# Kernel tuning notes

Hardware: AMD Instinct MI355X
Metric: run time of the kernel (lower is better)

## Reference

```python
import jax, jax.numpy as jnp
import numpy as np

KERNEL = (3, 3, 3)
STRIDE = (1, 1, 1)
PAD = (1, 1, 1)
DIL = (1, 1, 1)


def setup_inputs() -> dict:
    key = jax.random.key(0)
    k1, k2 = jax.random.split(key)
    # input: [B, C, D, H, W]
    x = jax.random.normal(k1, (2, 64, 16, 64, 64), dtype=jnp.float32)
    # per-pixel weights: [B, heads, weight_channels, kernel_volume, D_out, H_out, W_out]
    weight = jax.random.normal(k2, (2, 1, 16, 27, 16, 64, 64), dtype=jnp.float32)
    return {"x": x, "weight": weight}


def _aggregate(x, weight):
    # involution-style 3D local aggregation with zero padding.
    B, C, D, H, W = x.shape
    _, heads, wc, kvol, Do, Ho, Wo = weight.shape
    kd, kh, kw = KERNEL
    assert kvol == kd * kh * kw and C % wc == 0
    Q = C // wc  # channel-sharing groups: channel c uses weight channel c % wc
    xp = jnp.pad(x, ((0, 0), (0, 0), (PAD[0], PAD[0]), (PAD[1], PAD[1]), (PAD[2], PAD[2])))
    # channels laid out so that c = q*wc + r -> weight channel r == c % wc
    out = jnp.zeros((B, heads, Q, wc, Do, Ho, Wo), dtype=x.dtype)
    for ikd in range(kd):
        for ikh in range(kh):
            for ikw in range(kw):  # fixed small structural loop (27 taps)
                k = (ikd * kh + ikh) * kw + ikw
                d0 = ikd * DIL[0]
                h0 = ikh * DIL[1]
                w0 = ikw * DIL[2]
                x_k = xp[:, :,
                         d0:d0 + (Do - 1) * STRIDE[0] + 1:STRIDE[0],
                         h0:h0 + (Ho - 1) * STRIDE[1] + 1:STRIDE[1],
                         w0:w0 + (Wo - 1) * STRIDE[2] + 1:STRIDE[2]]
                x_k = x_k.reshape(B, Q, wc, Do, Ho, Wo)
                # [B,1,Q,wc,Do,Ho,Wo] * [B,heads,1,wc,Do,Ho,Wo]
                out = out + x_k[:, None] * weight[:, :, None, :, k]
    return out.reshape(B, heads * C, Do, Ho, Wo)


def reference(x, weight):
    return _aggregate(x, weight)
```

## Files before the change

kernel.cpp:

```cpp
#include <hip/hip_runtime.h>


#define D_DIM 16
#define NQ 4
#define RS 68

typedef float f4_t __attribute__((ext_vector_type(4)));

__global__ __launch_bounds__(256) void lconv_kernel(
    const float* __restrict__ x, const float* __restrict__ wt, float* __restrict__ out)
{
    __shared__ __align__(16) float lds[2][NQ][18][RS];

    const int tid = threadIdx.x;
    const int tw  = tid & 15;
    const int th  = tid >> 4;

    int bid = blockIdx.x;
    const int ho_tile = bid & 3;  bid >>= 2;
    const int dout    = bid & 15; bid >>= 4;
    const int c       = bid & 15; bid >>= 4;
    const int b       = bid;

    const int ho_base = ho_tile * 16;
    const int ho  = ho_base + th;
    const int wo0 = tw * 4;
    const int lw  = (tw == 0) ? 65 : (wo0 - 1);

    {
        float* l0 = &lds[0][0][0][0];
        for (int i = tid; i < 2 * NQ * 18 * 4; i += 256) {
            const int word = 64 + (i & 3);
            const int idx  = i >> 2;
            l0[(size_t)idx * RS + word] = 0.f;
        }
        const int oob_h = (ho_tile == 0) ? 0 : (ho_tile == 3) ? 17 : -1;
        if (oob_h >= 0) {
            for (int i = tid; i < 2 * NQ * RS; i += 256) {
                const int bq = i / RS, w = i - bq * RS;
                l0[((size_t)bq * 18 + oob_h) * RS + w] = 0.f;
            }
        }
    }

    const float* xbase = x + ((size_t)(b * 64 + c) * 16) * 4096;

    auto stage = [&](int buf, int d) {
        const float* src = xbase + (size_t)d * 4096;
        for (int i = tid; i < 72 * 16; i += 256) {
            const int row = i >> 4;
            const int seg = i & 15;
            const int q   = row / 18;
            const int hl  = row - q * 18;
            const int gh  = ho_base - 1 + hl;
            if ((unsigned)gh < 64u) {
                const f4_t v = *reinterpret_cast<const f4_t*>(
                    src + (size_t)q * 1048576 + (size_t)gh * 64 + seg * 4);
                *reinterpret_cast<f4_t*>(&lds[buf][q][hl][seg * 4]) = v;
            }
        }
    };

    float acc[NQ][4];
    #pragma unroll
    for (int q = 0; q < NQ; ++q)
        #pragma unroll
        for (int j = 0; j < 4; ++j) acc[q][j] = 0.f;

    const float* wbase = wt + (((size_t)(b * 16 + c) * 27) * 16 + dout) * 4096
                            + (size_t)ho * 64 + wo0;

    if (dout - 1 >= 0) stage(0, dout - 1);
    __syncthreads();

    #pragma unroll
    for (int dd = 0; dd < 3; ++dd) {
        const int cur = dd & 1, nxt = cur ^ 1;
        const int dn = dout + dd;
        if (dd < 2 && dn < D_DIM) stage(nxt, dn);

        const int d = dout + dd - 1;
        if ((unsigned)d < (unsigned)D_DIM) {
            #pragma unroll
            for (int dh = 0; dh < 3; ++dh) {
                float xv[NQ][6];
                #pragma unroll
                for (int q = 0; q < NQ; ++q) {
                    const float* r = &lds[cur][q][th + dh][0];
                    const f4_t m = *reinterpret_cast<const f4_t*>(r + wo0);
                    xv[q][0] = r[lw];
                    xv[q][1] = m.x; xv[q][2] = m.y; xv[q][3] = m.z; xv[q][4] = m.w;
                    xv[q][5] = r[wo0 + 4];
                }
                #pragma unroll
                for (int dw = 0; dw < 3; ++dw) {
                    const int k = (dd * 3 + dh) * 3 + dw;
                    const f4_t w4 = __builtin_nontemporal_load(
                        reinterpret_cast<const f4_t*>(wbase + (size_t)k * 65536));
                    #pragma unroll
                    for (int q = 0; q < NQ; ++q) {
                        acc[q][0] = fmaf(xv[q][0 + dw], w4.x, acc[q][0]);
                        acc[q][1] = fmaf(xv[q][1 + dw], w4.y, acc[q][1]);
                        acc[q][2] = fmaf(xv[q][2 + dw], w4.z, acc[q][2]);
                        acc[q][3] = fmaf(xv[q][3 + dw], w4.w, acc[q][3]);
                    }
                }
            }
        }
        __syncthreads();
    }

    #pragma unroll
    for (int q = 0; q < NQ; ++q) {
        float* orow = out + ((size_t)(b * 64 + q * 16 + c) * 16 + dout) * 4096
                          + (size_t)ho * 64 + wo0;
        f4_t r; r.x = acc[q][0]; r.y = acc[q][1]; r.z = acc[q][2]; r.w = acc[q][3];
        __builtin_nontemporal_store(r, reinterpret_cast<f4_t*>(orow));
    }
}

extern "C" void kernel_launch(void* const* d_in, const int* in_sizes, int n_in,
                              void* d_out, int out_size, void* d_ws, size_t ws_size,
                              hipStream_t stream) {
    const float* x  = (const float*)d_in[0];
    const float* wt = (const float*)d_in[1];
    float* out      = (float*)d_out;

    dim3 grid(2048), block(256);
    hipLaunchKernelGGL(lconv_kernel, grid, block, 0, stream, x, wt, out);
}
```

Measured before the change: 59.49 us.

## Process four output depths per block with ring-buffered async LDS staging

Each block now computes four consecutive output depth slices, staging input depth planes into a four-slot LDS ring so each plane is loaded once and reused across three output depths. Staging uses global_load_lds async copies, and out-of-range rows and depths read from a zeroed workspace page set by a memset before launch. This cuts the grid from 2048 to 512 blocks and roughly halves redundant input loads, but it lowers the number of resident waves available to hide the dominant per-pixel weight streaming, and it adds a memset to each launch.

```diff
diff --git a/kernel.cpp b/kernel.cpp
--- a/kernel.cpp
+++ b/kernel.cpp
@@ -1,16 +1,24 @@
 #include <hip/hip_runtime.h>
+#include <stdint.h>
 
 
-#define D_DIM 16
 #define NQ 4
-#define RS 68
-
 typedef float f4_t __attribute__((ext_vector_type(4)));
 
+#define BUF_FLOATS (4 * 18 * 64)
+#define LDS_FLOATS (64 + 4 * BUF_FLOATS + 64)
+
+__device__ __forceinline__ void async_copy16(const float* gsrc, float* ldst) {
+    __builtin_amdgcn_global_load_lds(
+        (const __attribute__((address_space(1))) uint32_t*)gsrc,
+        (__attribute__((address_space(3))) uint32_t*)ldst, 16, 0, 0);
+}
+
 __global__ __launch_bounds__(256) void lconv_kernel(
-    const float* __restrict__ x, const float* __restrict__ wt, float* __restrict__ out)
+    const float* __restrict__ x, const float* __restrict__ wt, float* __restrict__ out,
+    const float* __restrict__ zp)
 {
-    __shared__ __align__(16) float lds[2][NQ][18][RS];
+    __shared__ float lds_raw[LDS_FLOATS];
 
     const int tid = threadIdx.x;
     const int tw  = tid & 15;
@@ -18,79 +26,71 @@
 
     int bid = blockIdx.x;
     const int ho_tile = bid & 3;  bid >>= 2;
-    const int dout    = bid & 15; bid >>= 4;
+    const int a       = bid & 3;  bid >>= 2;
     const int c       = bid & 15; bid >>= 4;
     const int b       = bid;
 
     const int ho_base = ho_tile * 16;
     const int ho  = ho_base + th;
     const int wo0 = tw * 4;
-    const int lw  = (tw == 0) ? 65 : (wo0 - 1);
-
-    {
-        float* l0 = &lds[0][0][0][0];
-        for (int i = tid; i < 2 * NQ * 18 * 4; i += 256) {
-            const int word = 64 + (i & 3);
-            const int idx  = i >> 2;
-            l0[(size_t)idx * RS + word] = 0.f;
-        }
-        const int oob_h = (ho_tile == 0) ? 0 : (ho_tile == 3) ? 17 : -1;
-        if (oob_h >= 0) {
-            for (int i = tid; i < 2 * NQ * RS; i += 256) {
-                const int bq = i / RS, w = i - bq * RS;
-                l0[((size_t)bq * 18 + oob_h) * RS + w] = 0.f;
-            }
-        }
-    }
+    const int d0  = a * 4;
 
     const float* xbase = x + ((size_t)(b * 64 + c) * 16) * 4096;
 
-    auto stage = [&](int buf, int d) {
-        const float* src = xbase + (size_t)d * 4096;
-        for (int i = tid; i < 72 * 16; i += 256) {
-            const int row = i >> 4;
-            const int seg = i & 15;
-            const int q   = row / 18;
-            const int hl  = row - q * 18;
-            const int gh  = ho_base - 1 + hl;
-            if ((unsigned)gh < 64u) {
-                const f4_t v = *reinterpret_cast<const f4_t*>(
-                    src + (size_t)q * 1048576 + (size_t)gh * 64 + seg * 4);
-                *reinterpret_cast<f4_t*>(&lds[buf][q][hl][seg * 4]) = v;
+    auto stage = [&](int d) {
+        const int buf   = (d + 1) & 3;
+        const bool dok  = ((unsigned)d < 16u);
+        float* dbase    = &lds_raw[64 + buf * BUF_FLOATS];
+        #pragma unroll
+        for (int it = 0; it < 5; ++it) {
+            const int i = it * 256 + tid;
+            if (i < 1152) {
+                const int row = i >> 4;
+                const int seg = i & 15;
+                const int q   = row / 18;
+                const int hl  = row - q * 18;
+                const int gh  = ho_base - 1 + hl;
+                const bool ok = dok && ((unsigned)gh < 64u);
+                const float* src = ok
+                    ? (xbase + (size_t)q * 1048576 + (size_t)d * 4096 + (size_t)gh * 64 + seg * 4)
+                    : (zp + seg * 4);
+                async_copy16(src, dbase + i * 4);
             }
         }
     };
 
-    float acc[NQ][4];
-    #pragma unroll
-    for (int q = 0; q < NQ; ++q)
-        #pragma unroll
-        for (int j = 0; j < 4; ++j) acc[q][j] = 0.f;
-
-    const float* wbase = wt + (((size_t)(b * 16 + c) * 27) * 16 + dout) * 4096
-                            + (size_t)ho * 64 + wo0;
-
-    if (dout - 1 >= 0) stage(0, dout - 1);
+    stage(d0 - 1);
+    stage(d0);
+    stage(d0 + 1);
     __syncthreads();
 
-    #pragma unroll
-    for (int dd = 0; dd < 3; ++dd) {
-        const int cur = dd & 1, nxt = cur ^ 1;
-        const int dn = dout + dd;
-        if (dd < 2 && dn < D_DIM) stage(nxt, dn);
+    for (int dd4 = 0; dd4 < 4; ++dd4) {
+        const int dout = d0 + dd4;
+        if (dd4 < 3) stage(dout + 2);
 
-        const int d = dout + dd - 1;
-        if ((unsigned)d < (unsigned)D_DIM) {
+        const float* wbase = wt + (((size_t)(b * 16 + c) * 27) * 16 + dout) * 4096
+                                + (size_t)ho * 64 + wo0;
+
+        float acc[NQ][4];
+        #pragma unroll
+        for (int q = 0; q < NQ; ++q)
+            #pragma unroll
+            for (int j = 0; j < 4; ++j) acc[q][j] = 0.f;
+
+        #pragma unroll
+        for (int dd = 0; dd < 3; ++dd) {
+            const int buf = (dout + dd) & 3;
+            const float* bbase = &lds_raw[64 + buf * BUF_FLOATS];
             #pragma unroll
             for (int dh = 0; dh < 3; ++dh) {
                 float xv[NQ][6];
                 #pragma unroll
                 for (int q = 0; q < NQ; ++q) {
-                    const float* r = &lds[cur][q][th + dh][0];
+                    const float* r = bbase + (q * 18 + th + dh) * 64;
                     const f4_t m = *reinterpret_cast<const f4_t*>(r + wo0);
-                    xv[q][0] = r[lw];
+                    xv[q][0] = (tw > 0)  ? r[wo0 - 1] : 0.f;
                     xv[q][1] = m.x; xv[q][2] = m.y; xv[q][3] = m.z; xv[q][4] = m.w;
-                    xv[q][5] = r[wo0 + 4];
+                    xv[q][5] = (tw < 15) ? r[wo0 + 4] : 0.f;
                 }
                 #pragma unroll
                 for (int dw = 0; dw < 3; ++dw) {
@@ -107,15 +107,16 @@
                 }
             }
         }
+
+        #pragma unroll
+        for (int q = 0; q < NQ; ++q) {
+            float* orow = out + ((size_t)(b * 64 + q * 16 + c) * 16 + dout) * 4096
+                              + (size_t)ho * 64 + wo0;
+            f4_t rr; rr.x = acc[q][0]; rr.y = acc[q][1]; rr.z = acc[q][2]; rr.w = acc[q][3];
+            __builtin_nontemporal_store(rr, reinterpret_cast<f4_t*>(orow));
+        }
+
         __syncthreads();
-    }
-
-    #pragma unroll
-    for (int q = 0; q < NQ; ++q) {
-        float* orow = out + ((size_t)(b * 64 + q * 16 + c) * 16 + dout) * 4096
-                          + (size_t)ho * 64 + wo0;
-        f4_t r; r.x = acc[q][0]; r.y = acc[q][1]; r.z = acc[q][2]; r.w = acc[q][3];
-        __builtin_nontemporal_store(r, reinterpret_cast<f4_t*>(orow));
     }
 }
 
@@ -126,6 +127,9 @@
     const float* wt = (const float*)d_in[1];
     float* out      = (float*)d_out;
 
-    dim3 grid(2048), block(256);
-    hipLaunchKernelGGL(lconv_kernel, grid, block, 0, stream, x, wt, out);
+    hipMemsetAsync(d_ws, 0, 4096, stream);
+
+    dim3 grid(512), block(256);
+    hipLaunchKernelGGL(lconv_kernel, grid, block, 0, stream, x, wt, out,
+                       (const float*)d_ws);
 }
```

Result: slower. 63.36 us (+6.5%).
